# Performance work log

Hardware: AMD Instinct MI355X
Metric: run time of the kernel (lower is better)

The kernel has to match this reference:

```python
import jax, jax.numpy as jnp
import numpy as np

N_NODES = 50000
N_EDGES = 600000


def gcn_conv(x, src, dst, W, b, num_nodes):
    # x: [N, Cin] -> [N, Cout]; symmetric-normalized GCN with self-loops
    h = x @ W  # [N, Cout]
    loop = jnp.arange(num_nodes, dtype=src.dtype)
    s = jnp.concatenate([src, loop])
    d = jnp.concatenate([dst, loop])
    ones = jnp.ones(s.shape[0], dtype=h.dtype)
    deg = jax.ops.segment_sum(ones, d, num_segments=num_nodes)  # in-degree incl self-loop
    dinv = jnp.where(deg > 0, jax.lax.rsqrt(deg), 0.0)
    norm = dinv[s] * dinv[d]  # [E+N]
    msg = h[s] * norm[:, None]  # gather + scale
    out = jax.ops.segment_sum(msg, d, num_segments=num_nodes)  # scatter-add
    return out + b


def setup_inputs() -> dict:
    key = jax.random.key(0)
    k1, k2, k3, k4 = jax.random.split(key, 4)
    x = jax.random.normal(k1, (N_NODES, 128), dtype=jnp.float32)
    edge_index = jax.random.randint(k2, (2, N_EDGES), 0, N_NODES, dtype=jnp.int64)
    W1 = jax.random.normal(k3, (128, 128), dtype=jnp.float32) * (1.0 / np.sqrt(128))
    b1 = jnp.zeros((128,), dtype=jnp.float32)
    W2 = jax.random.normal(k4, (128, 64), dtype=jnp.float32) * (1.0 / np.sqrt(128))
    b2 = jnp.zeros((64,), dtype=jnp.float32)
    return {"x": x, "edge_index": edge_index, "W1": W1, "b1": b1, "W2": W2, "b2": b2}


def reference(x, edge_index, W1, b1, W2, b2):
    src, dst = edge_index[0], edge_index[1]
    h = gcn_conv(x, src, dst, W1, b1, N_NODES)
    h = jax.nn.relu(h)
    out = gcn_conv(h, src, dst, W2, b2, N_NODES)
    return out
```

## Files before the change

kernel.cpp:

```cpp
#include <hip/hip_runtime.h>
#include <cstddef>
#include <cstdint>

#define N_NODES 50000
#define N_EDGES 600000
#define M_TILES 3125
#define GEMM_BLKS 782
#define NBUCK 196
#define BUCK_CAP 4096
#define K1_BLKS 147
#define K1_EDGES 4096

typedef short bf16x8 __attribute__((ext_vector_type(8)));
typedef float f32x4 __attribute__((ext_vector_type(4)));


__device__ __forceinline__ unsigned short f32_to_bf16(float x) {
  unsigned u = __float_as_uint(x);
  u += 0x7FFFu + ((u >> 16) & 1u);
  return (unsigned short)(u >> 16);
}
__device__ __forceinline__ float bf16_to_f32(unsigned short h) {
  return __uint_as_float((unsigned)h << 16);
}
__device__ __forceinline__ float bf16_lo(unsigned g) {
  return __uint_as_float(g << 16);
}
__device__ __forceinline__ float bf16_hi(unsigned g) {
  return __uint_as_float(g & 0xFFFF0000u);
}

__device__ __forceinline__ void split8(const float* __restrict__ p, bf16x8& hi,
                                       bf16x8& lo) {
  const float4 v0 = *(const float4*)p;
  const float4 v1 = *(const float4*)(p + 4);
  float v[8] = {v0.x, v0.y, v0.z, v0.w, v1.x, v1.y, v1.z, v1.w};
#pragma unroll
  for (int i = 0; i < 8; i++) {
    const unsigned short h = f32_to_bf16(v[i]);
    hi[i] = (short)h;
    lo[i] = (short)f32_to_bf16(v[i] - bf16_to_f32(h));
  }
}

__global__ __launch_bounds__(256) void k_prep(
    const float* __restrict__ W1, const float* __restrict__ W2,
    unsigned short* __restrict__ w1h, unsigned short* __restrict__ w1l,
    unsigned short* __restrict__ w2h, unsigned short* __restrict__ w2l,
    int* __restrict__ cursor) {
  const int b = blockIdx.x;
  const int tid = threadIdx.x;
  if (b < 96) {
    const int i = b * 256 + tid;
    const float* W;
    unsigned short *wh, *wl;
    int o, cout;
    if (i < 16384) {
      W = W1; wh = w1h; wl = w1l; o = i; cout = 128;
    } else {
      W = W2; wh = w2h; wl = w2l; o = i - 16384; cout = 64;
    }
    const int j = o & 7;
    const int lane = (o >> 3) & 63;
    const int t = o >> 9;
    const int ks = t & 3;
    const int ct = t >> 2;
    const int k = ks * 32 + (lane >> 4) * 8 + j;
    const int n = ct * 16 + (lane & 15);
    const float v = W[k * cout + n];
    const unsigned short h = f32_to_bf16(v);
    wh[o] = h;
    wl[o] = f32_to_bf16(v - bf16_to_f32(h));
  } else {
    if (tid < NBUCK) cursor[tid] = tid * BUCK_CAP;
  }
}

template <int COUT>
__device__ __forceinline__ void gemm_body(const int wtile, const int lane,
                                          const float* __restrict__ X,
                                          const unsigned short* __restrict__ Wph,
                                          const unsigned short* __restrict__ Wpl,
                                          unsigned short* __restrict__ Hs) {
  constexpr int CT = COUT / 16;
  const int m = lane & 15;
  const int q = lane >> 4;

  f32x4 acc[CT];
#pragma unroll
  for (int ct = 0; ct < CT; ct++) acc[ct] = {0.f, 0.f, 0.f, 0.f};

  const float* xp = X + (size_t)(wtile * 16 + m) * 128 + q * 8;

#pragma unroll
  for (int ks = 0; ks < 4; ks++) {
    bf16x8 ah, al;
    split8(xp + ks * 32, ah, al);
#pragma unroll
    for (int ct = 0; ct < CT; ct++) {
      const size_t bo = ((size_t)(ct * 4 + ks) * 64 + lane) * 8;
      const bf16x8 bh = *(const bf16x8*)(Wph + bo);
      const bf16x8 bl = *(const bf16x8*)(Wpl + bo);
      acc[ct] = __builtin_amdgcn_mfma_f32_16x16x32_bf16(ah, bh, acc[ct], 0, 0, 0);
      acc[ct] = __builtin_amdgcn_mfma_f32_16x16x32_bf16(al, bh, acc[ct], 0, 0, 0);
      acc[ct] = __builtin_amdgcn_mfma_f32_16x16x32_bf16(ah, bl, acc[ct], 0, 0, 0);
    }
  }
#pragma unroll
  for (int ct = 0; ct < CT; ct++) {
#pragma unroll
    for (int r = 0; r < 4; r++) {
      const int orow = wtile * 16 + q * 4 + r;
      Hs[(size_t)orow * COUT + ct * 16 + m] = f32_to_bf16(acc[ct][r]);
    }
  }
}

__global__ __launch_bounds__(256) void k_route_gemm128(
    const float* __restrict__ X, const unsigned short* __restrict__ Wph,
    const unsigned short* __restrict__ Wpl, unsigned short* __restrict__ Hs,
    const int* __restrict__ src, const int* __restrict__ dst,
    int* __restrict__ cursor, unsigned* __restrict__ routed) {
  __shared__ int hist[NBUCK];
  __shared__ int lcur[NBUCK];
  const int tid = threadIdx.x;
  if (blockIdx.x < K1_BLKS) {
    for (int t = tid; t < NBUCK; t += 256) hist[t] = 0;
    __syncthreads();
    unsigned packed[16];
    bool cvalid[4];
    const int base = blockIdx.x * K1_EDGES;
#pragma unroll
    for (int c = 0; c < 4; c++) {
      const int i4 = base + c * 1024 + tid * 4;
      cvalid[c] = (i4 < N_EDGES);
      if (cvalid[c]) {
        const int4 d4 = *(const int4*)(dst + i4);
        const int4 s4 = *(const int4*)(src + i4);
        packed[c * 4 + 0] = ((unsigned)d4.x << 16) | (unsigned)s4.x;
        packed[c * 4 + 1] = ((unsigned)d4.y << 16) | (unsigned)s4.y;
        packed[c * 4 + 2] = ((unsigned)d4.z << 16) | (unsigned)s4.z;
        packed[c * 4 + 3] = ((unsigned)d4.w << 16) | (unsigned)s4.w;
#pragma unroll
        for (int j = 0; j < 4; j++)
          atomicAdd(&hist[packed[c * 4 + j] >> 24], 1);
      }
    }
    __syncthreads();
    for (int t = tid; t < NBUCK; t += 256)
      lcur[t] = atomicAdd(&cursor[t], hist[t]);
    __syncthreads();
#pragma unroll
    for (int c = 0; c < 4; c++) {
      if (cvalid[c]) {
#pragma unroll
        for (int j = 0; j < 4; j++) {
          const unsigned pk = packed[c * 4 + j];
          const int slot = atomicAdd(&lcur[pk >> 24], 1);
          routed[slot] = pk;
        }
      }
    }
  } else {
    const int wtile = (blockIdx.x - K1_BLKS) * 4 + (tid >> 6);
    if (wtile < M_TILES) gemm_body<128>(wtile, tid & 63, X, Wph, Wpl, Hs);
  }
}

__global__ __launch_bounds__(1024) void k_bsort(
    const unsigned* __restrict__ routed, const int* __restrict__ cursor,
    int* __restrict__ counts, int* __restrict__ start,
    int* __restrict__ sorted_src) {
  __shared__ unsigned ebuf[BUCK_CAP];
  __shared__ int h2[256];
  __shared__ int c2[256];
  const int b = blockIdx.x;
  const int tid = threadIdx.x;
  const int n = cursor[b] - b * BUCK_CAP;
  for (int i = tid; i < n; i += 1024) ebuf[i] = routed[b * BUCK_CAP + i];
  if (tid < 256) h2[tid] = 0;
  __syncthreads();
  for (int i = tid; i < n; i += 1024)
    atomicAdd(&h2[(ebuf[i] >> 16) & 255], 1);
  __syncthreads();
  int own = 0;
  if (tid < 256) own = h2[tid];
  for (int s = 1; s < 256; s <<= 1) {
    int t = 0;
    if (tid < 256 && tid >= s) t = h2[tid - s];
    __syncthreads();
    if (tid < 256) h2[tid] += t;
    __syncthreads();
  }
  if (tid < 256) {
    const int pfx = h2[tid] - own;
    c2[tid] = pfx;
    const int d = b * 256 + tid;
    if (d < N_NODES) {
      counts[d] = own;
      start[d] = b * BUCK_CAP + pfx;
    }
  }
  __syncthreads();
  for (int i = tid; i < n; i += 1024) {
    const unsigned pk = ebuf[i];
    const int r = atomicAdd(&c2[(pk >> 16) & 255], 1);
    sorted_src[b * BUCK_CAP + r] = (int)(pk & 0xFFFFu);
  }
}

__global__ __launch_bounds__(256) void k_gemm64(
    const float* __restrict__ A1, const unsigned short* __restrict__ Wph,
    const unsigned short* __restrict__ Wpl, unsigned short* __restrict__ Hs) {
  const int wtile = blockIdx.x * 4 + (threadIdx.x >> 6);
  if (wtile < M_TILES) gemm_body<64>(wtile, threadIdx.x & 63, A1, Wph, Wpl, Hs);
}

__global__ __launch_bounds__(256) void k_agg128(
    const unsigned* __restrict__ Hb, const int* __restrict__ counts,
    const int* __restrict__ start, const int* __restrict__ sorted_src,
    const float* __restrict__ bias, float* __restrict__ a1) {
  const int lane = threadIdx.x & 63;
  const int v = blockIdx.x * 4 + (threadIdx.x >> 6);
  if (v >= N_NODES) return;
  const int deg = counts[v];
  const float dv = rsqrtf((float)deg + 1.0f);
  const int e0 = start[v];

  const unsigned gself = Hb[(size_t)v * 64 + lane];
  float ax = bf16_lo(gself) * (dv * dv);
  float ay = bf16_hi(gself) * (dv * dv);

  for (int base = 0; base < deg; base += 64) {
    const int cnt = min(64, deg - base);
    int si = 0;
    float wi = 0.f;
    if (base + lane < deg) {
      si = sorted_src[e0 + base + lane];
      wi = rsqrtf((float)counts[si] + 1.0f) * dv;
    }
    int j = 0;
    for (; j + 4 <= cnt; j += 4) {
      const int s0 = __shfl(si, j);
      const int s1 = __shfl(si, j + 1);
      const int s2 = __shfl(si, j + 2);
      const int s3 = __shfl(si, j + 3);
      const float w0 = __shfl(wi, j);
      const float w1 = __shfl(wi, j + 1);
      const float w2 = __shfl(wi, j + 2);
      const float w3 = __shfl(wi, j + 3);
      const unsigned g0 = Hb[(size_t)s0 * 64 + lane];
      const unsigned g1 = Hb[(size_t)s1 * 64 + lane];
      const unsigned g2 = Hb[(size_t)s2 * 64 + lane];
      const unsigned g3 = Hb[(size_t)s3 * 64 + lane];
      ax += bf16_lo(g0) * w0; ay += bf16_hi(g0) * w0;
      ax += bf16_lo(g1) * w1; ay += bf16_hi(g1) * w1;
      ax += bf16_lo(g2) * w2; ay += bf16_hi(g2) * w2;
      ax += bf16_lo(g3) * w3; ay += bf16_hi(g3) * w3;
    }
    for (; j < cnt; j++) {
      const int s = __shfl(si, j);
      const float w = __shfl(wi, j);
      const unsigned g = Hb[(size_t)s * 64 + lane];
      ax += bf16_lo(g) * w;
      ay += bf16_hi(g) * w;
    }
  }
  const float2 b = ((const float2*)bias)[lane];
  float2 r;
  r.x = fmaxf(ax + b.x, 0.f);
  r.y = fmaxf(ay + b.y, 0.f);
  ((float2*)a1)[(size_t)v * 64 + lane] = r;
}

__global__ __launch_bounds__(256) void k_agg64(
    const unsigned* __restrict__ Hb, const int* __restrict__ counts,
    const int* __restrict__ start, const int* __restrict__ sorted_src,
    const float* __restrict__ bias, float* __restrict__ out) {
  const int hl = threadIdx.x & 31;
  const int v = blockIdx.x * 8 + (threadIdx.x >> 5);
  if (v >= N_NODES) return;
  const int deg = counts[v];
  const float dv = rsqrtf((float)deg + 1.0f);
  const int e0 = start[v];

  const unsigned gself = Hb[(size_t)v * 32 + hl];
  float ax = bf16_lo(gself) * (dv * dv);
  float ay = bf16_hi(gself) * (dv * dv);

  for (int base = 0; base < deg; base += 32) {
    const int cnt = min(32, deg - base);
    int si = 0;
    float wi = 0.f;
    if (base + hl < deg) {
      si = sorted_src[e0 + base + hl];
      wi = rsqrtf((float)counts[si] + 1.0f) * dv;
    }
    int j = 0;
    for (; j + 4 <= cnt; j += 4) {
      const int s0 = __shfl(si, j, 32);
      const int s1 = __shfl(si, j + 1, 32);
      const int s2 = __shfl(si, j + 2, 32);
      const int s3 = __shfl(si, j + 3, 32);
      const float w0 = __shfl(wi, j, 32);
      const float w1 = __shfl(wi, j + 1, 32);
      const float w2 = __shfl(wi, j + 2, 32);
      const float w3 = __shfl(wi, j + 3, 32);
      const unsigned g0 = Hb[(size_t)s0 * 32 + hl];
      const unsigned g1 = Hb[(size_t)s1 * 32 + hl];
      const unsigned g2 = Hb[(size_t)s2 * 32 + hl];
      const unsigned g3 = Hb[(size_t)s3 * 32 + hl];
      ax += bf16_lo(g0) * w0; ay += bf16_hi(g0) * w0;
      ax += bf16_lo(g1) * w1; ay += bf16_hi(g1) * w1;
      ax += bf16_lo(g2) * w2; ay += bf16_hi(g2) * w2;
      ax += bf16_lo(g3) * w3; ay += bf16_hi(g3) * w3;
    }
    for (; j < cnt; j++) {
      const int s = __shfl(si, j, 32);
      const float w = __shfl(wi, j, 32);
      const unsigned g = Hb[(size_t)s * 32 + hl];
      ax += bf16_lo(g) * w;
      ay += bf16_hi(g) * w;
    }
  }
  const float2 b = ((const float2*)bias)[hl];
  float2 r;
  r.x = ax + b.x;
  r.y = ay + b.y;
  ((float2*)out)[(size_t)v * 32 + hl] = r;
}


extern "C" void kernel_launch(void* const* d_in, const int* in_sizes, int n_in,
                              void* d_out, int out_size, void* d_ws, size_t ws_size,
                              hipStream_t stream) {
  const float* x = (const float*)d_in[0];
  const int* ei = (const int*)d_in[1];
  const float* W1 = (const float*)d_in[2];
  const float* b1 = (const float*)d_in[3];
  const float* W2 = (const float*)d_in[4];
  const float* b2 = (const float*)d_in[5];
  const int* src = ei;
  const int* dst = ei + N_EDGES;

  char* p = (char*)d_ws;
  auto alloc = [&](size_t bytes) {
    char* q = p;
    p += (bytes + 255) & ~(size_t)255;
    return q;
  };
  int* cursor = (int*)alloc((size_t)NBUCK * 4);
  unsigned* routed = (unsigned*)alloc((size_t)NBUCK * BUCK_CAP * 4);
  int* sorted_src = (int*)alloc((size_t)NBUCK * BUCK_CAP * 4);
  int* counts = (int*)alloc((size_t)N_NODES * 4);
  int* start = (int*)alloc((size_t)N_NODES * 4);
  unsigned short* w1h = (unsigned short*)alloc(16384 * 2);
  unsigned short* w1l = (unsigned short*)alloc(16384 * 2);
  unsigned short* w2h = (unsigned short*)alloc(8192 * 2);
  unsigned short* w2l = (unsigned short*)alloc(8192 * 2);
  unsigned short* h1b = (unsigned short*)alloc((size_t)N_NODES * 128 * 2);
  float* a1 = (float*)alloc((size_t)N_NODES * 128 * 4);
  unsigned short* h2b = (unsigned short*)alloc((size_t)N_NODES * 64 * 2);

  hipLaunchKernelGGL(k_prep, dim3(97), dim3(256), 0, stream, W1, W2, w1h, w1l,
                     w2h, w2l, cursor);
  hipLaunchKernelGGL(k_route_gemm128, dim3(K1_BLKS + GEMM_BLKS), dim3(256), 0,
                     stream, x, w1h, w1l, h1b, src, dst, cursor, routed);
  hipLaunchKernelGGL(k_bsort, dim3(NBUCK), dim3(1024), 0, stream, routed,
                     cursor, counts, start, sorted_src);
  hipLaunchKernelGGL(k_agg128, dim3((N_NODES + 3) / 4), dim3(256), 0, stream,
                     (const unsigned*)h1b, counts, start, sorted_src, b1, a1);
  hipLaunchKernelGGL(k_gemm64, dim3(GEMM_BLKS), dim3(256), 0, stream, a1, w2h,
                     w2l, h2b);
  hipLaunchKernelGGL(k_agg64, dim3((N_NODES + 7) / 8), dim3(256), 0, stream,
                     (const unsigned*)h2b, counts, start, sorted_src, b2,
                     (float*)d_out);
}
```

Before: 165.6 us.

## Fuse layer-1 aggregation with layer-2 GEMM through shared memory

Merges the first aggregation kernel and the second-layer GEMM into one kernel. Each block aggregates 16 nodes into an LDS tile, then runs split-bf16 MFMA on that tile against W2. This drops the full fp32 a1 intermediate (writing and re-reading it from global memory) and one kernel launch. In exchange, blocks are smaller in work granularity and the GEMM phase waits on the slowest of the 16 aggregations in the block.

```diff
diff --git a/kernel.cpp b/kernel.cpp
--- a/kernel.cpp
+++ b/kernel.cpp
@@ -209,68 +209,88 @@
   }
 }
 
-__global__ __launch_bounds__(256) void k_gemm64(
-    const float* __restrict__ A1, const unsigned short* __restrict__ Wph,
-    const unsigned short* __restrict__ Wpl, unsigned short* __restrict__ Hs) {
-  const int wtile = blockIdx.x * 4 + (threadIdx.x >> 6);
-  if (wtile < M_TILES) gemm_body<64>(wtile, threadIdx.x & 63, A1, Wph, Wpl, Hs);
-}
-
-__global__ __launch_bounds__(256) void k_agg128(
+__global__ __launch_bounds__(256) void k_agg128_gemm64(
     const unsigned* __restrict__ Hb, const int* __restrict__ counts,
     const int* __restrict__ start, const int* __restrict__ sorted_src,
-    const float* __restrict__ bias, float* __restrict__ a1) {
+    const float* __restrict__ bias, const unsigned short* __restrict__ Wph,
+    const unsigned short* __restrict__ Wpl, unsigned short* __restrict__ Hs) {
+  __shared__ float a1s[16][132];
   const int lane = threadIdx.x & 63;
-  const int v = blockIdx.x * 4 + (threadIdx.x >> 6);
-  if (v >= N_NODES) return;
-  const int deg = counts[v];
-  const float dv = rsqrtf((float)deg + 1.0f);
-  const int e0 = start[v];
-
-  const unsigned gself = Hb[(size_t)v * 64 + lane];
-  float ax = bf16_lo(gself) * (dv * dv);
-  float ay = bf16_hi(gself) * (dv * dv);
-
-  for (int base = 0; base < deg; base += 64) {
-    const int cnt = min(64, deg - base);
-    int si = 0;
-    float wi = 0.f;
-    if (base + lane < deg) {
-      si = sorted_src[e0 + base + lane];
-      wi = rsqrtf((float)counts[si] + 1.0f) * dv;
-    }
-    int j = 0;
-    for (; j + 4 <= cnt; j += 4) {
-      const int s0 = __shfl(si, j);
-      const int s1 = __shfl(si, j + 1);
-      const int s2 = __shfl(si, j + 2);
-      const int s3 = __shfl(si, j + 3);
-      const float w0 = __shfl(wi, j);
-      const float w1 = __shfl(wi, j + 1);
-      const float w2 = __shfl(wi, j + 2);
-      const float w3 = __shfl(wi, j + 3);
-      const unsigned g0 = Hb[(size_t)s0 * 64 + lane];
-      const unsigned g1 = Hb[(size_t)s1 * 64 + lane];
-      const unsigned g2 = Hb[(size_t)s2 * 64 + lane];
-      const unsigned g3 = Hb[(size_t)s3 * 64 + lane];
-      ax += bf16_lo(g0) * w0; ay += bf16_hi(g0) * w0;
-      ax += bf16_lo(g1) * w1; ay += bf16_hi(g1) * w1;
-      ax += bf16_lo(g2) * w2; ay += bf16_hi(g2) * w2;
-      ax += bf16_lo(g3) * w3; ay += bf16_hi(g3) * w3;
-    }
-    for (; j < cnt; j++) {
-      const int s = __shfl(si, j);
-      const float w = __shfl(wi, j);
-      const unsigned g = Hb[(size_t)s * 64 + lane];
-      ax += bf16_lo(g) * w;
-      ay += bf16_hi(g) * w;
-    }
-  }
-  const float2 b = ((const float2*)bias)[lane];
-  float2 r;
-  r.x = fmaxf(ax + b.x, 0.f);
-  r.y = fmaxf(ay + b.y, 0.f);
-  ((float2*)a1)[(size_t)v * 64 + lane] = r;
+  const int wave = threadIdx.x >> 6;
+  const float2 bb = ((const float2*)bias)[lane];
+
+#pragma unroll
+  for (int i = 0; i < 4; i++) {
+    const int r = wave * 4 + i;
+    const int v = blockIdx.x * 16 + r;
+    const int deg = counts[v];
+    const float dv = rsqrtf((float)deg + 1.0f);
+    const int e0 = start[v];
+
+    const unsigned gself = Hb[(size_t)v * 64 + lane];
+    float ax = bf16_lo(gself) * (dv * dv);
+    float ay = bf16_hi(gself) * (dv * dv);
+
+    for (int base = 0; base < deg; base += 64) {
+      const int cnt = min(64, deg - base);
+      int si = 0;
+      float wi = 0.f;
+      if (base + lane < deg) {
+        si = sorted_src[e0 + base + lane];
+        wi = rsqrtf((float)counts[si] + 1.0f) * dv;
+      }
+      int j = 0;
+      for (; j + 4 <= cnt; j += 4) {
+        const int s0 = __shfl(si, j);
+        const int s1 = __shfl(si, j + 1);
+        const int s2 = __shfl(si, j + 2);
+        const int s3 = __shfl(si, j + 3);
+        const float w0 = __shfl(wi, j);
+        const float w1 = __shfl(wi, j + 1);
+        const float w2 = __shfl(wi, j + 2);
+        const float w3 = __shfl(wi, j + 3);
+        const unsigned g0 = Hb[(size_t)s0 * 64 + lane];
+        const unsigned g1 = Hb[(size_t)s1 * 64 + lane];
+        const unsigned g2 = Hb[(size_t)s2 * 64 + lane];
+        const unsigned g3 = Hb[(size_t)s3 * 64 + lane];
+        ax += bf16_lo(g0) * w0; ay += bf16_hi(g0) * w0;
+        ax += bf16_lo(g1) * w1; ay += bf16_hi(g1) * w1;
+        ax += bf16_lo(g2) * w2; ay += bf16_hi(g2) * w2;
+        ax += bf16_lo(g3) * w3; ay += bf16_hi(g3) * w3;
+      }
+      for (; j < cnt; j++) {
+        const int s = __shfl(si, j);
+        const float w = __shfl(wi, j);
+        const unsigned g = Hb[(size_t)s * 64 + lane];
+        ax += bf16_lo(g) * w;
+        ay += bf16_hi(g) * w;
+      }
+    }
+    a1s[r][lane * 2] = fmaxf(ax + bb.x, 0.f);
+    a1s[r][lane * 2 + 1] = fmaxf(ay + bb.y, 0.f);
+  }
+  __syncthreads();
+
+  const int ct = wave;
+  const int m = lane & 15;
+  const int q = lane >> 4;
+  f32x4 acc = {0.f, 0.f, 0.f, 0.f};
+#pragma unroll
+  for (int ks = 0; ks < 4; ks++) {
+    bf16x8 ah, al;
+    split8(&a1s[m][ks * 32 + q * 8], ah, al);
+    const size_t bo = ((size_t)(ct * 4 + ks) * 64 + lane) * 8;
+    const bf16x8 bh = *(const bf16x8*)(Wph + bo);
+    const bf16x8 bl = *(const bf16x8*)(Wpl + bo);
+    acc = __builtin_amdgcn_mfma_f32_16x16x32_bf16(ah, bh, acc, 0, 0, 0);
+    acc = __builtin_amdgcn_mfma_f32_16x16x32_bf16(al, bh, acc, 0, 0, 0);
+    acc = __builtin_amdgcn_mfma_f32_16x16x32_bf16(ah, bl, acc, 0, 0, 0);
+  }
+#pragma unroll
+  for (int r = 0; r < 4; r++) {
+    const int orow = blockIdx.x * 16 + q * 4 + r;
+    Hs[(size_t)orow * 64 + ct * 16 + m] = f32_to_bf16(acc[r]);
+  }
 }
 
 __global__ __launch_bounds__(256) void k_agg64(
@@ -359,7 +379,6 @@
   unsigned short* w2h = (unsigned short*)alloc(8192 * 2);
   unsigned short* w2l = (unsigned short*)alloc(8192 * 2);
   unsigned short* h1b = (unsigned short*)alloc((size_t)N_NODES * 128 * 2);
-  float* a1 = (float*)alloc((size_t)N_NODES * 128 * 4);
   unsigned short* h2b = (unsigned short*)alloc((size_t)N_NODES * 64 * 2);
 
   hipLaunchKernelGGL(k_prep, dim3(97), dim3(256), 0, stream, W1, W2, w1h, w1l,
@@ -368,9 +387,8 @@
                      stream, x, w1h, w1l, h1b, src, dst, cursor, routed);
   hipLaunchKernelGGL(k_bsort, dim3(NBUCK), dim3(1024), 0, stream, routed,
                      cursor, counts, start, sorted_src);
-  hipLaunchKernelGGL(k_agg128, dim3((N_NODES + 3) / 4), dim3(256), 0, stream,
-                     (const unsigned*)h1b, counts, start, sorted_src, b1, a1);
-  hipLaunchKernelGGL(k_gemm64, dim3(GEMM_BLKS), dim3(256), 0, stream, a1, w2h,
+  hipLaunchKernelGGL(k_agg128_gemm64, dim3(M_TILES), dim3(256), 0, stream,
+                     (const unsigned*)h1b, counts, start, sorted_src, b1, w2h,
                      w2l, h2b);
   hipLaunchKernelGGL(k_agg64, dim3((N_NODES + 7) / 8), dim3(256), 0, stream,
                      (const unsigned*)h2b, counts, start, sorted_src, b2,
```

New measurement: 158.7 us. -4.2%, faster.
